# Kernel optimization log

Measured on AMD Instinct MI355X. Metric: run time of the kernel, lower is better.

The kernel has to match this reference:

```python
import jax, jax.numpy as jnp
import numpy as np

B, S, HID = 2, 2048, 2048
H = 16
Q_LORA = 1536
KV_LORA = 512
NOPE = 128
ROPE = 64
VDIM = 128
EPS = 1e-6
THETA = 10000.0
SCALE = 1.0 / np.sqrt(NOPE + ROPE)


def rmsnorm(x, w):
    var = jnp.mean(jnp.square(x), axis=-1, keepdims=True)
    return x * jax.lax.rsqrt(var + EPS) * w


def rotate_half(x):
    x1, x2 = jnp.split(x, 2, axis=-1)
    return jnp.concatenate([-x2, x1], axis=-1)


def setup_inputs() -> dict:
    key = jax.random.key(0)
    ks = jax.random.split(key, 10)
    w = 0.02
    hidden_states = jax.random.normal(ks[0], (B, S, HID), jnp.float32)
    # causal additive mask (bsz, 1, q_len, kv_len)
    causal = jnp.tril(jnp.ones((S, S), jnp.bool_))
    attention_mask = jnp.where(causal, 0.0, jnp.finfo(jnp.float32).min)[None, None].repeat(B, 0)
    position_ids = jnp.broadcast_to(jnp.arange(S, dtype=jnp.int64), (B, S))
    return {
        'hidden_states': hidden_states,
        'attention_mask': attention_mask,
        'q_a_w': jax.random.normal(ks[1], (Q_LORA, HID), jnp.float32) * w,
        'q_a_ln_w': jnp.ones((Q_LORA,), jnp.float32),
        'q_b_rope_w': jax.random.normal(ks[2], (H * ROPE, Q_LORA), jnp.float32) * w,
        'qk_nope_w': jax.random.normal(ks[3], (H * KV_LORA, Q_LORA), jnp.float32) * w,
        'kv_a_w': jax.random.normal(ks[4], (KV_LORA + ROPE, HID), jnp.float32) * w,
        'kv_a_ln_w': jnp.ones((KV_LORA,), jnp.float32),
        'v_b_w': jax.random.normal(ks[5], (H * VDIM, KV_LORA), jnp.float32) * w,
        'o_w': jax.random.normal(ks[6], (HID, H * VDIM), jnp.float32) * w,
        'position_ids': position_ids,
    }


def reference(hidden_states, attention_mask, q_a_w, q_a_ln_w, q_b_rope_w, qk_nope_w,
              kv_a_w, kv_a_ln_w, v_b_w, o_w, position_ids):
    b, s, _ = hidden_states.shape
    # low-rank Q path
    q_a = rmsnorm(hidden_states @ q_a_w.T, q_a_ln_w)                 # (b,s,Q_LORA)
    q_rope = (q_a @ q_b_rope_w.T).reshape(b, s, H, ROPE).transpose(0, 2, 1, 3)  # (b,h,s,rd)
    # compressed KV + shared rope key
    ckv_full = hidden_states @ kv_a_w.T                              # (b,s,KV_LORA+ROPE)
    ckv = rmsnorm(ckv_full[..., :KV_LORA], kv_a_ln_w)                # (b,s,KV_LORA)
    k_rope = ckv_full[..., KV_LORA:]                                 # (b,s,rd)
    # rotary embedding
    inv_freq = 1.0 / (THETA ** (jnp.arange(0, ROPE, 2, dtype=jnp.float32) / ROPE))
    t = jnp.arange(s, dtype=jnp.float32)
    freqs = jnp.outer(t, inv_freq)                                   # (s, rd/2)
    emb = jnp.concatenate([freqs, freqs], axis=-1)                   # (s, rd)
    cos = jnp.cos(emb)[position_ids][:, None]                        # (b,1,s,rd)
    sin = jnp.sin(emb)[position_ids][:, None]
    q_rope = q_rope * cos + rotate_half(q_rope) * sin                # (b,h,s,rd)
    k_rope = k_rope[:, None] * cos + rotate_half(k_rope[:, None]) * sin  # (b,1,s,rd)
    # absorbed nope score: q_a -> (b,h,s,KV_LORA) then vs compressed kv
    nope_q = (q_a @ qk_nope_w.T).reshape(b, s, H, KV_LORA).transpose(0, 2, 1, 3)
    nope_score = jnp.einsum('bhqc,bkc->bhqk', nope_q, ckv)
    rope_score = jnp.einsum('bhqr,bkr->bhqk', q_rope, k_rope[:, 0])
    attn = (nope_score + rope_score) * SCALE + attention_mask
    attn = jax.nn.softmax(attn.astype(jnp.float32), axis=-1).astype(hidden_states.dtype)
    # AV in compressed space, then absorbed v projection
    ctx = jnp.einsum('bhqk,bkc->bhqc', attn, ckv)                    # (b,h,q,KV_LORA)
    v_w = v_b_w.reshape(H, VDIM, KV_LORA)
    out = jnp.einsum('bhqc,hvc->bhqv', ctx, v_w)                     # (b,h,q,VDIM)
    out = out.transpose(0, 2, 1, 3).reshape(b, s, H * VDIM)
    return out @ o_w.T
```

## Files before the change

### kernel.cpp

```cpp
#include <hip/hip_runtime.h>
#include <hip/hip_bf16.h>

typedef __bf16 bf16;
typedef __bf16 bf16x8 __attribute__((ext_vector_type(8)));
typedef float f32x4 __attribute__((ext_vector_type(4)));
typedef float f32x16 __attribute__((ext_vector_type(16)));

#define AS3(p) ((__attribute__((address_space(3))) void*)(p))
#define AS1(p) ((const __attribute__((address_space(1))) void*)(p))
#define GLDS16(g,l) __builtin_amdgcn_global_load_lds(AS1(g), AS3(l), 16, 0, 0)
#define MFMA_BF16(a,b,c) __builtin_amdgcn_mfma_f32_16x16x32_bf16((a),(b),(c),0,0,0)
#define MFMA32(a,b,c) __builtin_amdgcn_mfma_f32_32x32x16_bf16((a),(b),(c),0,0,0)

constexpr int S_ = 2048;
constexpr int H_ = 16;
constexpr int KVL_ = 512;
constexpr int ROPE_ = 64;
constexpr int VD_ = 128;
constexpr int DQK_ = 576;
constexpr int QKV_N = 2176;
constexpr float SCALE_ = 0.07216878364870323f;

__device__ __forceinline__ bf16 to_bf16(float f) {
    unsigned u = __builtin_bit_cast(unsigned, f);
    unsigned r = u + 0x7FFFu + ((u >> 16) & 1u);
    unsigned short h = (unsigned short)(r >> 16);
    return __builtin_bit_cast(bf16, h);
}

__device__ __forceinline__ unsigned cvt_pk_bf16(float lo, float hi) {
    unsigned r;
    asm("v_cvt_pk_bf16_f32 %0, %1, %2" : "=v"(r) : "v"(lo), "v"(hi));
    return r;
}

__global__ void cast_kernel(const float* __restrict__ in, bf16* __restrict__ out, long n, long pad) {
    long i = ((long)blockIdx.x * 256 + threadIdx.x) * 4;
    long stride = (long)gridDim.x * 256 * 4;
    for (; i < pad; i += stride) {
        if (i < n) {
            float4 v = *(const float4*)(in + i);
            out[i + 0] = to_bf16(v.x);
            out[i + 1] = to_bf16(v.y);
            out[i + 2] = to_bf16(v.z);
            out[i + 3] = to_bf16(v.w);
        } else {
            out[i + 0] = to_bf16(0.f); out[i + 1] = to_bf16(0.f);
            out[i + 2] = to_bf16(0.f); out[i + 3] = to_bf16(0.f);
        }
    }
}

__global__ void rmsnorm_kernel(const float* __restrict__ in, const float* __restrict__ w,
                               bf16* __restrict__ out, int dim, int istride) {
    const int row = blockIdx.x;
    const float* x = in + (long)row * istride;
    float ss = 0.f;
    for (int i = threadIdx.x; i < dim; i += 256) { float v = x[i]; ss += v * v; }
#pragma unroll
    for (int d = 1; d < 64; d <<= 1) ss += __shfl_xor(ss, d);
    __shared__ float red[4];
    if ((threadIdx.x & 63) == 0) red[threadIdx.x >> 6] = ss;
    __syncthreads();
    float tot = red[0] + red[1] + red[2] + red[3];
    float rs = rsqrtf(tot / (float)dim + 1e-6f);
    for (int i = threadIdx.x; i < dim; i += 256)
        out[(long)row * dim + i] = to_bf16(x[i] * rs * w[i]);
}

__global__ void rope_table_kernel(float* __restrict__ cosT, float* __restrict__ sinT) {
    int idx = blockIdx.x * 256 + threadIdx.x;
    if (idx >= S_ * 32) return;
    int s = idx >> 5, j = idx & 31;
    float invf = expf(-(float)(2 * j) * (1.0f / 64.0f) * 9.210340371976184f);
    float a = (float)s * invf;
    cosT[idx] = cosf(a);
    sinT[idx] = sinf(a);
}

__global__ void rope_q_kernel(const float* __restrict__ qp, const float* __restrict__ cosT,
                              const float* __restrict__ sinT, bf16* __restrict__ out) {
    long bs = blockIdx.x;
    int s = (int)(bs & (S_ - 1));
    for (int e = threadIdx.x; e < H_ * ROPE_; e += 256) {
        int hh = e >> 6, i = e & 63;
        const float* x = qp + bs * (H_ * ROPE_) + hh * 64;
        float other = (i < 32) ? -x[i + 32] : x[i - 32];
        float c = cosT[s * 32 + (i & 31)], sn = sinT[s * 32 + (i & 31)];
        out[bs * (H_ * ROPE_) + e] = to_bf16((x[i] * c + other * sn) * SCALE_);
    }
}

__global__ void rope_k_kernel(const float* __restrict__ ckvf, const float* __restrict__ cosT,
                              const float* __restrict__ sinT, bf16* __restrict__ out) {
    long bs = blockIdx.x;
    int i = threadIdx.x;
    int s = (int)(bs & (S_ - 1));
    const float* x = ckvf + bs * QKV_N + 2048;
    float other = (i < 32) ? -x[i + 32] : x[i - 32];
    float c = cosT[s * 32 + (i & 31)], sn = sinT[s * 32 + (i & 31)];
    out[bs * 64 + i] = to_bf16(x[i] * c + other * sn);
}

template <int MODE>
__global__ __launch_bounds__(256, 2)
void gemm_bt_kernel(const bf16* __restrict__ A, const bf16* __restrict__ Bm,
                    void* __restrict__ Cout, int M, int N, int K) {
    constexpr int BK = 32;
    __shared__ bf16 As[128 * BK];
    __shared__ bf16 Bs[128 * BK];
    const int tid = threadIdx.x;
    const int w = tid >> 6;
    const int lane = tid & 63;
    const int nwg = gridDim.x * gridDim.y;
    const int lin = blockIdx.y * gridDim.x + blockIdx.x;
    const int swz = (lin & 7) * (nwg >> 3) + (lin >> 3);
    const long m0 = (long)(swz % gridDim.x) * 128;
    const long n0 = (long)(swz / gridDim.x) * 128;
    const int wm = (w >> 1) * 64, wn = (w & 1) * 64;
    const int lr = lane & 15;
    const int lk = (lane >> 4) * 8;

    const int c0 = w * 2, c1 = w * 2 + 1;
    const int srow0 = c0 * 16 + (lane >> 2);
    const int srow1 = c1 * 16 + (lane >> 2);
    const int skc = (lane & 3) * 8;
    const bf16* ga0 = A + (m0 + srow0) * (long)K + skc;
    const bf16* ga1 = A + (m0 + srow1) * (long)K + skc;
    const bf16* gb0 = Bm + (n0 + srow0) * (long)K + skc;
    const bf16* gb1 = Bm + (n0 + srow1) * (long)K + skc;

    f32x4 acc[4][4] = {};
    for (int kk = 0; kk < K; kk += BK) {
        __syncthreads();
        GLDS16(ga0, &As[c0 * 512]);
        GLDS16(gb0, &Bs[c0 * 512]);
        GLDS16(ga1, &As[c1 * 512]);
        GLDS16(gb1, &Bs[c1 * 512]);
        ga0 += BK; ga1 += BK; gb0 += BK; gb1 += BK;
        __syncthreads();
        bf16x8 av[4], bv[4];
#pragma unroll
        for (int i = 0; i < 4; i++) av[i] = *(const bf16x8*)&As[(wm + i * 16 + lr) * BK + lk];
#pragma unroll
        for (int j = 0; j < 4; j++) bv[j] = *(const bf16x8*)&Bs[(wn + j * 16 + lr) * BK + lk];
#pragma unroll
        for (int i = 0; i < 4; i++)
#pragma unroll
            for (int j = 0; j < 4; j++)
                acc[i][j] = MFMA_BF16(av[i], bv[j], acc[i][j]);
    }
    const int r4 = (lane >> 4) * 4;
#pragma unroll
    for (int i = 0; i < 4; i++)
#pragma unroll
        for (int j = 0; j < 4; j++) {
            long gmb = m0 + wm + i * 16 + r4;
            long gn = n0 + wn + j * 16 + lr;
#pragma unroll
            for (int r = 0; r < 4; r++) {
                long gm = gmb + r;
                float v = acc[i][j][r];
                if (MODE == 0) {
                    if (gn < N) ((float*)Cout)[gm * N + gn] = v;
                } else if (MODE == 1) {
                    if (gn < N) ((bf16*)Cout)[gm * N + gn] = to_bf16(v * SCALE_);
                } else {
                    long idx = (gm >> 11) * (2048L * 2048) + gn * 2048 + (gm & 2047);
                    ((bf16*)Cout)[idx] = to_bf16(v);
                }
            }
        }
}

__global__ __launch_bounds__(256, 2)
void flash_kernel(const bf16* __restrict__ nopeq, const bf16* __restrict__ ropeq,
                  const bf16* __restrict__ ckv, const bf16* __restrict__ krope,
                  const bf16* __restrict__ vt, bf16* __restrict__ outa) {
    __shared__ bf16 Ks2[32 * 512];
    __shared__ bf16 Krs[32 * 64];
    __shared__ char VtsB[10240];
    __shared__ char PldsB[4][32 * 80];
    const int tid = threadIdx.x;
    const int w = tid >> 6, lane = tid & 63;
    const int l31 = lane & 31;
    const int hi = lane >> 5;
    const int kel = hi * 8;
    const int klo = hi * 16;
    const int h = blockIdx.y, b = blockIdx.z;
    const int xq = (b == 0) ? (int)blockIdx.x : (15 - (int)blockIdx.x);
    const int q0 = xq * 128;
    const long bS = (long)b * S_;
    const int qg = q0 + (l31 << 2) + w;
    const int kvoff = hi * 4;

    bf16x8 qf[36];
    {
        const bf16* np = nopeq + (bS + qg) * (long)(H_ * KVL_) + h * KVL_;
        const bf16* rp = ropeq + (bS + qg) * (long)(H_ * ROPE_) + h * ROPE_;
#pragma unroll
        for (int t = 0; t < 32; ++t) qf[t] = *(const bf16x8*)(np + t * 16 + kel);
#pragma unroll
        for (int t = 0; t < 4; ++t) qf[32 + t] = *(const bf16x8*)(rp + t * 16 + kel);
    }

    unsigned soff[12];
#pragma unroll
    for (int k = 0; k < 8; ++k) {
        int c = w + 4 * k;
        soff[k] = (unsigned)((bS + c) * 1024 + ((lane * 16) ^ ((c & 7) << 4)));
    }
    {
        int rr = w * 8 + (lane >> 3);
        soff[8] = (unsigned)((bS + rr) * 128 + (((lane & 7) * 16) ^ ((rr & 7) << 4)));
    }
#pragma unroll
    for (int k = 9; k < 12; ++k) {
        int cc = (k == 11) ? (8 + w) : (w + 4 * (k - 9));
        int byt = cc * 1024 + lane * 16;
        int v = byt / 80, col = byt - v * 80;
        soff[k] = (col < 64) ? (unsigned)((((long)(b * H_ + h) * VD_ + v) * S_ + (col >> 1)) * 2) : 0u;
    }

    f32x16 accv[4] = {};
    float m_run = -3e38f, l_run = 0.f;
    const int nkv = q0 / 32 + 4;
    const int kswz = (l31 & 7) << 4;

    for (int it = 0; it < nkv; ++it) {
        const int kv0 = it * 32;
        __syncthreads();
#pragma unroll
        for (int k = 0; k < 8; ++k) {
            GLDS16((const char*)ckv + soff[k], (char*)Ks2 + (w + 4 * k) * 1024);
            soff[k] += 32768;
        }
        GLDS16((const char*)krope + soff[8], (char*)Krs + w * 1024);
        soff[8] += 4096;
        GLDS16((const char*)vt + soff[9], VtsB + w * 1024); soff[9] += 64;
        GLDS16((const char*)vt + soff[10], VtsB + (w + 4) * 1024); soff[10] += 64;
        if (w < 2) { GLDS16((const char*)vt + soff[11], VtsB + (8 + w) * 1024); soff[11] += 64; }
        __syncthreads();

        f32x16 sc = {};
        __builtin_amdgcn_s_setprio(1);
#pragma unroll
        for (int t = 0; t < 32; ++t) {
            bf16x8 kf = *(const bf16x8*)((const char*)Ks2 + l31 * 1024 + ((t * 32 + klo) ^ kswz));
            sc = MFMA32(kf, qf[t], sc);
        }
#pragma unroll
        for (int t = 0; t < 4; ++t) {
            bf16x8 kf = *(const bf16x8*)((const char*)Krs + l31 * 128 + ((t * 32 + klo) ^ kswz));
            sc = MFMA32(kf, qf[32 + t], sc);
        }
        __builtin_amdgcn_s_setprio(0);

        float s[16];
        if (kv0 + 31 > q0 + w) {
#pragma unroll
            for (int r = 0; r < 16; ++r) {
                int kvg = kv0 + kvoff + ((r & 3) + 8 * (r >> 2));
                s[r] = (kvg > qg) ? -3e38f : sc[r];
            }
        } else {
#pragma unroll
            for (int r = 0; r < 16; ++r) s[r] = sc[r];
        }

        float m8[8];
#pragma unroll
        for (int r = 0; r < 8; ++r) m8[r] = fmaxf(s[r], s[r + 8]);
        float m4a = fmaxf(m8[0], m8[1]), m4b = fmaxf(m8[2], m8[3]);
        float m4c = fmaxf(m8[4], m8[5]), m4d = fmaxf(m8[6], m8[7]);
        float mx = fmaxf(fmaxf(m4a, m4b), fmaxf(m4c, m4d));
        mx = fmaxf(mx, __shfl_xor(mx, 32));

        float mnew = fmaxf(m_run, mx);
        float corr = __expf(m_run - mnew);
#pragma unroll
        for (int r = 0; r < 16; ++r) s[r] = __expf(s[r] - mnew);
        float r8[8];
#pragma unroll
        for (int r = 0; r < 8; ++r) r8[r] = s[r] + s[r + 8];
        float r4a = r8[0] + r8[1], r4b = r8[2] + r8[3], r4c = r8[4] + r8[5], r4d = r8[6] + r8[7];
        float rs = (r4a + r4b) + (r4c + r4d);
        rs += __shfl_xor(rs, 32);

        if (__any(mnew > m_run)) {
#pragma unroll
            for (int vg = 0; vg < 4; ++vg)
#pragma unroll
                for (int r = 0; r < 16; ++r) accv[vg][r] *= corr;
        }
        l_run = l_run * corr + rs;
        m_run = mnew;

        {
            char* prow = PldsB[w] + l31 * 80;
#pragma unroll
            for (int g = 0; g < 4; ++g) {
                uint2 pk;
                pk.x = cvt_pk_bf16(s[4 * g + 0], s[4 * g + 1]);
                pk.y = cvt_pk_bf16(s[4 * g + 2], s[4 * g + 3]);
                *(uint2*)(prow + g * 16 + 8 * hi) = pk;
            }
        }
        bf16x8 pfrag[2];
#pragma unroll
        for (int c = 0; c < 2; ++c)
            pfrag[c] = *(const bf16x8*)(PldsB[w] + l31 * 80 + c * 32 + klo);

        __builtin_amdgcn_s_setprio(1);
#pragma unroll
        for (int c = 0; c < 2; ++c) {
#pragma unroll
            for (int vg = 0; vg < 4; ++vg) {
                bf16x8 vf = *(const bf16x8*)(VtsB + (vg * 32 + l31) * 80 + c * 32 + klo);
                accv[vg] = MFMA32(vf, pfrag[c], accv[vg]);
            }
        }
        __builtin_amdgcn_s_setprio(0);
    }

    float invl = 1.f / l_run;
    bf16* orow = outa + (bS + qg) * (long)(H_ * VD_) + h * VD_;
#pragma unroll
    for (int vg = 0; vg < 4; ++vg)
#pragma unroll
        for (int rq = 0; rq < 4; ++rq) {
            int vb = vg * 32 + rq * 8 + kvoff;
            ushort4 u;
            u.x = __builtin_bit_cast(unsigned short, to_bf16(accv[vg][rq * 4 + 0] * invl));
            u.y = __builtin_bit_cast(unsigned short, to_bf16(accv[vg][rq * 4 + 1] * invl));
            u.z = __builtin_bit_cast(unsigned short, to_bf16(accv[vg][rq * 4 + 2] * invl));
            u.w = __builtin_bit_cast(unsigned short, to_bf16(accv[vg][rq * 4 + 3] * invl));
            *(ushort4*)(orow + vb) = u;
        }
}

extern "C" void kernel_launch(void* const* d_in, const int* in_sizes, int n_in,
                              void* d_out, int out_size, void* d_ws, size_t ws_size,
                              hipStream_t stream) {
    const float* hidden     = (const float*)d_in[0];
    const float* q_a_w      = (const float*)d_in[2];
    const float* q_a_ln_w   = (const float*)d_in[3];
    const float* q_b_rope_w = (const float*)d_in[4];
    const float* qk_nope_w  = (const float*)d_in[5];
    const float* kv_a_w     = (const float*)d_in[6];
    const float* kv_a_ln_w  = (const float*)d_in[7];
    const float* v_b_w      = (const float*)d_in[8];
    const float* o_w        = (const float*)d_in[9];

    char* ws = (char*)d_ws;
    size_t off = 0;
    auto alloc = [&](size_t bytes) -> void* {
        void* p = ws + off;
        off += (bytes + 255) & ~(size_t)255;
        return p;
    };
    bf16* hb     = (bf16*)alloc(4096L * 2048 * 2);
    bf16* wqakv  = (bf16*)alloc((long)QKV_N * 2048 * 2);
    bf16* wqr    = (bf16*)alloc(1024L * 1536 * 2);
    bf16* wnp    = (bf16*)alloc(8192L * 1536 * 2);
    bf16* wvb    = (bf16*)alloc(2048L * 512 * 2);
    bf16* wo     = (bf16*)alloc(2048L * 2048 * 2);
    float* f32scr = (float*)alloc(4096L * QKV_N * 4);
    bf16* qab    = (bf16*)alloc(4096L * 1536 * 2);
    bf16* qrb    = (bf16*)alloc(4096L * 1024 * 2);
    bf16* npq    = (bf16*)alloc(4096L * 8192 * 2);
    bf16* ckvb   = (bf16*)alloc(4096L * 512 * 2);
    bf16* krb    = (bf16*)alloc(4096L * 64 * 2);
    bf16* vtb    = (bf16*)alloc(2L * 2048 * 2048 * 2);
    bf16* aout   = (bf16*)alloc(4096L * 2048 * 2);
    float* cosT  = (float*)alloc(2048L * 32 * 4);
    float* sinT  = (float*)alloc(2048L * 32 * 4);
    (void)ws_size; (void)in_sizes; (void)n_in; (void)out_size;

    cast_kernel<<<1024, 256, 0, stream>>>(hidden, hb, 8388608L, 8388608L);
    cast_kernel<<<512, 256, 0, stream>>>(q_a_w, wqakv, 3145728L, 3145728L);
    cast_kernel<<<256, 256, 0, stream>>>(kv_a_w, wqakv + 1536L * 2048, 1179648L, 1310720L);
    cast_kernel<<<256, 256, 0, stream>>>(q_b_rope_w, wqr, 1572864L, 1572864L);
    cast_kernel<<<1024, 256, 0, stream>>>(qk_nope_w, wnp, 12582912L, 12582912L);
    cast_kernel<<<128, 256, 0, stream>>>(v_b_w, wvb, 1048576L, 1048576L);
    cast_kernel<<<512, 256, 0, stream>>>(o_w, wo, 4194304L, 4194304L);
    rope_table_kernel<<<256, 256, 0, stream>>>(cosT, sinT);

    gemm_bt_kernel<0><<<dim3(32, 17), 256, 0, stream>>>(hb, wqakv, f32scr, 4096, QKV_N, 2048);
    rmsnorm_kernel<<<4096, 256, 0, stream>>>(f32scr, q_a_ln_w, qab, 1536, QKV_N);
    rmsnorm_kernel<<<4096, 256, 0, stream>>>(f32scr + 1536, kv_a_ln_w, ckvb, 512, QKV_N);
    rope_k_kernel<<<4096, 64, 0, stream>>>(f32scr, cosT, sinT, krb);
    gemm_bt_kernel<0><<<dim3(32, 8), 256, 0, stream>>>(qab, wqr, f32scr, 4096, 1024, 1536);
    rope_q_kernel<<<4096, 256, 0, stream>>>(f32scr, cosT, sinT, qrb);
    gemm_bt_kernel<1><<<dim3(32, 64), 256, 0, stream>>>(qab, wnp, npq, 4096, 8192, 1536);
    gemm_bt_kernel<2><<<dim3(32, 16), 256, 0, stream>>>(ckvb, wvb, vtb, 4096, 2048, 512);
    flash_kernel<<<dim3(16, 16, 2), 256, 0, stream>>>(npq, qrb, ckvb, krb, vtb, aout);
    gemm_bt_kernel<0><<<dim3(32, 16), 256, 0, stream>>>(aout, wo, (float*)d_out, 4096, 2048, 2048);
}
```

Before: 608.6 us.

## Merge cast launches, fuse rmsnorm/rope-k, and double-buffer GEMM LDS

Replaces seven separate fp32-to-bf16 cast launches with one 2D-grid kernel indexed by segment. Fuses the two rmsnorm kernels and the rope-k kernel into a single per-row kernel, so the fp32 scratch row is read in one pass with fewer launches. Double-buffers the GEMM shared-memory tiles so the next K-tile's global-to-LDS load is issued before the current tile's MFMAs, with one barrier per iteration instead of two. This doubles LDS use per block and relies on the single trailing barrier to order the async LDS writes.

```diff
diff --git a/kernel.cpp b/kernel.cpp
--- a/kernel.cpp
+++ b/kernel.cpp
@@ -34,38 +34,33 @@
     return r;
 }
 
-__global__ void cast_kernel(const float* __restrict__ in, bf16* __restrict__ out, long n, long pad) {
+__global__ void cast_all_kernel(const float* __restrict__ s0, const float* __restrict__ s1,
+                                const float* __restrict__ s2, const float* __restrict__ s3,
+                                const float* __restrict__ s4, const float* __restrict__ s5,
+                                const float* __restrict__ s6,
+                                bf16* __restrict__ d0, bf16* __restrict__ d1, bf16* __restrict__ d2,
+                                bf16* __restrict__ d3, bf16* __restrict__ d4, bf16* __restrict__ d5,
+                                bf16* __restrict__ d6) {
+    constexpr long ns[7]  = {8388608L, 3145728L, 1179648L, 1572864L, 12582912L, 1048576L, 4194304L};
+    constexpr long pds[7] = {8388608L, 3145728L, 1310720L, 1572864L, 12582912L, 1048576L, 4194304L};
+    const int seg = blockIdx.y;
+    const float* in = (seg == 0) ? s0 : (seg == 1) ? s1 : (seg == 2) ? s2 : (seg == 3) ? s3
+                    : (seg == 4) ? s4 : (seg == 5) ? s5 : s6;
+    bf16* out = (seg == 0) ? d0 : (seg == 1) ? d1 : (seg == 2) ? d2 : (seg == 3) ? d3
+              : (seg == 4) ? d4 : (seg == 5) ? d5 : d6;
+    const long n = ns[seg], pad = pds[seg];
     long i = ((long)blockIdx.x * 256 + threadIdx.x) * 4;
-    long stride = (long)gridDim.x * 256 * 4;
+    const long stride = (long)gridDim.x * 256 * 4;
     for (; i < pad; i += stride) {
         if (i < n) {
             float4 v = *(const float4*)(in + i);
-            out[i + 0] = to_bf16(v.x);
-            out[i + 1] = to_bf16(v.y);
-            out[i + 2] = to_bf16(v.z);
-            out[i + 3] = to_bf16(v.w);
+            out[i + 0] = to_bf16(v.x); out[i + 1] = to_bf16(v.y);
+            out[i + 2] = to_bf16(v.z); out[i + 3] = to_bf16(v.w);
         } else {
             out[i + 0] = to_bf16(0.f); out[i + 1] = to_bf16(0.f);
             out[i + 2] = to_bf16(0.f); out[i + 3] = to_bf16(0.f);
         }
     }
-}
-
-__global__ void rmsnorm_kernel(const float* __restrict__ in, const float* __restrict__ w,
-                               bf16* __restrict__ out, int dim, int istride) {
-    const int row = blockIdx.x;
-    const float* x = in + (long)row * istride;
-    float ss = 0.f;
-    for (int i = threadIdx.x; i < dim; i += 256) { float v = x[i]; ss += v * v; }
-#pragma unroll
-    for (int d = 1; d < 64; d <<= 1) ss += __shfl_xor(ss, d);
-    __shared__ float red[4];
-    if ((threadIdx.x & 63) == 0) red[threadIdx.x >> 6] = ss;
-    __syncthreads();
-    float tot = red[0] + red[1] + red[2] + red[3];
-    float rs = rsqrtf(tot / (float)dim + 1e-6f);
-    for (int i = threadIdx.x; i < dim; i += 256)
-        out[(long)row * dim + i] = to_bf16(x[i] * rs * w[i]);
 }
 
 __global__ void rope_table_kernel(float* __restrict__ cosT, float* __restrict__ sinT) {
@@ -76,6 +71,36 @@
     float a = (float)s * invf;
     cosT[idx] = cosf(a);
     sinT[idx] = sinf(a);
+}
+
+__global__ void fused_post_kernel(const float* __restrict__ scr, const float* __restrict__ qw,
+                                  const float* __restrict__ kw, const float* __restrict__ cosT,
+                                  const float* __restrict__ sinT, bf16* __restrict__ qab,
+                                  bf16* __restrict__ ckvb, bf16* __restrict__ krb) {
+    const int row = blockIdx.x;
+    const int tid = threadIdx.x;
+    const float* x = scr + (long)row * QKV_N;
+    float ssq = 0.f, ssk = 0.f;
+    for (int i = tid; i < 1536; i += 256) { float v = x[i]; ssq += v * v; }
+    for (int i = tid; i < 512; i += 256) { float v = x[1536 + i]; ssk += v * v; }
+#pragma unroll
+    for (int d = 1; d < 64; d <<= 1) { ssq += __shfl_xor(ssq, d); ssk += __shfl_xor(ssk, d); }
+    __shared__ float rq[4], rk[4];
+    if ((tid & 63) == 0) { rq[tid >> 6] = ssq; rk[tid >> 6] = ssk; }
+    __syncthreads();
+    float rsq = rsqrtf((rq[0] + rq[1] + rq[2] + rq[3]) / 1536.f + 1e-6f);
+    float rsk = rsqrtf((rk[0] + rk[1] + rk[2] + rk[3]) / 512.f + 1e-6f);
+    for (int i = tid; i < 1536; i += 256)
+        qab[(long)row * 1536 + i] = to_bf16(x[i] * rsq * qw[i]);
+    for (int i = tid; i < 512; i += 256)
+        ckvb[(long)row * 512 + i] = to_bf16(x[1536 + i] * rsk * kw[i]);
+    if (tid < 64) {
+        int s = row & (S_ - 1);
+        const float* kr = x + 2048;
+        float other = (tid < 32) ? -kr[tid + 32] : kr[tid - 32];
+        float c = cosT[s * 32 + (tid & 31)], sn = sinT[s * 32 + (tid & 31)];
+        krb[(long)row * 64 + tid] = to_bf16(kr[tid] * c + other * sn);
+    }
 }
 
 __global__ void rope_q_kernel(const float* __restrict__ qp, const float* __restrict__ cosT,
@@ -91,24 +116,13 @@
     }
 }
 
-__global__ void rope_k_kernel(const float* __restrict__ ckvf, const float* __restrict__ cosT,
-                              const float* __restrict__ sinT, bf16* __restrict__ out) {
-    long bs = blockIdx.x;
-    int i = threadIdx.x;
-    int s = (int)(bs & (S_ - 1));
-    const float* x = ckvf + bs * QKV_N + 2048;
-    float other = (i < 32) ? -x[i + 32] : x[i - 32];
-    float c = cosT[s * 32 + (i & 31)], sn = sinT[s * 32 + (i & 31)];
-    out[bs * 64 + i] = to_bf16(x[i] * c + other * sn);
-}
-
 template <int MODE>
 __global__ __launch_bounds__(256, 2)
 void gemm_bt_kernel(const bf16* __restrict__ A, const bf16* __restrict__ Bm,
                     void* __restrict__ Cout, int M, int N, int K) {
     constexpr int BK = 32;
-    __shared__ bf16 As[128 * BK];
-    __shared__ bf16 Bs[128 * BK];
+    __shared__ bf16 As[2][128 * BK];
+    __shared__ bf16 Bs[2][128 * BK];
     const int tid = threadIdx.x;
     const int w = tid >> 6;
     const int lane = tid & 63;
@@ -130,26 +144,37 @@
     const bf16* gb0 = Bm + (n0 + srow0) * (long)K + skc;
     const bf16* gb1 = Bm + (n0 + srow1) * (long)K + skc;
 
+#define GSTAGE(p) do { \
+    GLDS16(ga0, &As[p][c0 * 512]); \
+    GLDS16(gb0, &Bs[p][c0 * 512]); \
+    GLDS16(ga1, &As[p][c1 * 512]); \
+    GLDS16(gb1, &Bs[p][c1 * 512]); \
+    ga0 += BK; ga1 += BK; gb0 += BK; gb1 += BK; \
+} while (0)
+
     f32x4 acc[4][4] = {};
-    for (int kk = 0; kk < K; kk += BK) {
-        __syncthreads();
-        GLDS16(ga0, &As[c0 * 512]);
-        GLDS16(gb0, &Bs[c0 * 512]);
-        GLDS16(ga1, &As[c1 * 512]);
-        GLDS16(gb1, &Bs[c1 * 512]);
-        ga0 += BK; ga1 += BK; gb0 += BK; gb1 += BK;
-        __syncthreads();
+    const int nT = K / BK;
+
+    GSTAGE(0);
+    __syncthreads();
+
+    for (int t = 0; t < nT; ++t) {
+        const int p = t & 1;
+        if (t + 1 < nT) GSTAGE(p ^ 1);
         bf16x8 av[4], bv[4];
 #pragma unroll
-        for (int i = 0; i < 4; i++) av[i] = *(const bf16x8*)&As[(wm + i * 16 + lr) * BK + lk];
-#pragma unroll
-        for (int j = 0; j < 4; j++) bv[j] = *(const bf16x8*)&Bs[(wn + j * 16 + lr) * BK + lk];
+        for (int i = 0; i < 4; i++) av[i] = *(const bf16x8*)&As[p][(wm + i * 16 + lr) * BK + lk];
+#pragma unroll
+        for (int j = 0; j < 4; j++) bv[j] = *(const bf16x8*)&Bs[p][(wn + j * 16 + lr) * BK + lk];
 #pragma unroll
         for (int i = 0; i < 4; i++)
 #pragma unroll
             for (int j = 0; j < 4; j++)
                 acc[i][j] = MFMA_BF16(av[i], bv[j], acc[i][j]);
-    }
+        __syncthreads();
+    }
+#undef GSTAGE
+
     const int r4 = (lane >> 4) * 4;
 #pragma unroll
     for (int i = 0; i < 4; i++)
@@ -377,19 +402,13 @@
     float* sinT  = (float*)alloc(2048L * 32 * 4);
     (void)ws_size; (void)in_sizes; (void)n_in; (void)out_size;
 
-    cast_kernel<<<1024, 256, 0, stream>>>(hidden, hb, 8388608L, 8388608L);
-    cast_kernel<<<512, 256, 0, stream>>>(q_a_w, wqakv, 3145728L, 3145728L);
-    cast_kernel<<<256, 256, 0, stream>>>(kv_a_w, wqakv + 1536L * 2048, 1179648L, 1310720L);
-    cast_kernel<<<256, 256, 0, stream>>>(q_b_rope_w, wqr, 1572864L, 1572864L);
-    cast_kernel<<<1024, 256, 0, stream>>>(qk_nope_w, wnp, 12582912L, 12582912L);
-    cast_kernel<<<128, 256, 0, stream>>>(v_b_w, wvb, 1048576L, 1048576L);
-    cast_kernel<<<512, 256, 0, stream>>>(o_w, wo, 4194304L, 4194304L);
+    cast_all_kernel<<<dim3(512, 7), 256, 0, stream>>>(
+        hidden, q_a_w, kv_a_w, q_b_rope_w, qk_nope_w, v_b_w, o_w,
+        hb, wqakv, wqakv + 1536L * 2048, wqr, wnp, wvb, wo);
     rope_table_kernel<<<256, 256, 0, stream>>>(cosT, sinT);
 
     gemm_bt_kernel<0><<<dim3(32, 17), 256, 0, stream>>>(hb, wqakv, f32scr, 4096, QKV_N, 2048);
-    rmsnorm_kernel<<<4096, 256, 0, stream>>>(f32scr, q_a_ln_w, qab, 1536, QKV_N);
-    rmsnorm_kernel<<<4096, 256, 0, stream>>>(f32scr + 1536, kv_a_ln_w, ckvb, 512, QKV_N);
-    rope_k_kernel<<<4096, 64, 0, stream>>>(f32scr, cosT, sinT, krb);
+    fused_post_kernel<<<4096, 256, 0, stream>>>(f32scr, q_a_ln_w, kv_a_ln_w, cosT, sinT, qab, ckvb, krb);
     gemm_bt_kernel<0><<<dim3(32, 8), 256, 0, stream>>>(qab, wqr, f32scr, 4096, 1024, 1536);
     rope_q_kernel<<<4096, 256, 0, stream>>>(f32scr, cosT, sinT, qrb);
     gemm_bt_kernel<1><<<dim3(32, 64), 256, 0, stream>>>(qab, wnp, npq, 4096, 8192, 1536);
```

Result: faster. 589.2 us (-3.2%).
